# Optimization experiments

Hardware: AMD Instinct MI355X
Metric: run time of the kernel (lower is better)

The kernel has to match this reference:

```python
import jax, jax.numpy as jnp
import numpy as np

D = 2            # n_angles (torus T^2)
NEURONS = 256
EPS = 1e-4       # PD regularizer on inertia matrix / Cholesky diagonal


def setup_inputs() -> dict:
    key = jax.random.key(0)
    ks = jax.random.split(key, 12)
    n = 131072
    d = D
    n_off = d * (d - 1) // 2
    x = jax.random.normal(ks[0], (n, 3 * d), dtype=jnp.float32)
    t = jnp.zeros((), dtype=jnp.float32)

    def lin(k, fan_in, fan_out):
        s = 1.0 / np.sqrt(fan_in)
        kw, kb = jax.random.split(k)
        W = jax.random.uniform(kw, (fan_in, fan_out), jnp.float32, -s, s)
        b = jax.random.uniform(kb, (fan_out,), jnp.float32, -s, s)
        return W, b

    W0, b0 = lin(ks[1], 2 * d, NEURONS)      # trunk layer 1 (input = angle embedding)
    W1, b1 = lin(ks[2], NEURONS, NEURONS)    # trunk layer 2
    Wd, bd = lin(ks[3], NEURONS, d)          # Cholesky diagonal head
    Wo, bo = lin(ks[4], NEURONS, n_off)      # Cholesky off-diagonal head
    Wv, bv = lin(ks[5], NEURONS, 1)          # potential energy head
    return {"t": t, "x": x, "W0": W0, "b0": b0, "W1": W1, "b1": b1,
            "Wd": Wd, "bd": bd, "Wo": Wo, "bo": bo, "Wv": Wv, "bv": bv}


def reference(t, x, W0, b0, W1, b1, Wd, bd, Wo, bo, Wv, bv):
    n = x.shape[0]
    d = x.shape[1] // 3
    q, q_dot, tau = jnp.split(x, [d, 2 * d], axis=1)
    di = jnp.diag_indices(d)
    ti = jnp.tril_indices(d, -1)
    eye = jnp.eye(d, dtype=x.dtype)

    def rigid_body(qi):  # qi: (d,) -> H (d,d) PD, V scalar
        emb = jnp.concatenate([jnp.cos(qi), jnp.sin(qi)])  # angle embedding (2d,)
        h = jnp.tanh(emb @ W0 + b0)
        h = jnp.tanh(h @ W1 + b1)
        l_diag = jax.nn.softplus(h @ Wd + bd) + EPS
        l_off = h @ Wo + bo
        V = (h @ Wv + bv)[0]
        L = jnp.zeros((d, d), x.dtype).at[di].set(l_diag).at[ti].set(l_off)
        H = L @ L.T + EPS * eye
        return H, V

    def dyn(qi, qdi, taui):
        H, _ = rigid_body(qi)
        # Coriolis: dHv/dq @ q_dot - d(0.5 q_dot^T H q_dot)/dq
        Hv_field = jax.jacfwd(lambda qq: rigid_body(qq)[0] @ qdi)(qi)        # (d, d)
        KE_field = jax.grad(lambda qq: 0.5 * qdi @ (rigid_body(qq)[0] @ qdi))(qi)
        C = Hv_field @ qdi - KE_field
        g = jax.grad(lambda qq: rigid_body(qq)[1])(qi)                        # dV/dq
        return jnp.linalg.solve(H, taui - C - g)                              # H qdd = rhs

    q_ddot = jax.vmap(dyn)(q, q_dot, tau)  # (n, d)
    return jnp.concatenate([q_dot, q_ddot, jnp.zeros_like(q_dot)], axis=1)
```

## Files before the change

kernel.cpp:

```cpp
#include <hip/hip_runtime.h>
#include <math.h>

#define SB 32
#define NTHREADS 512

typedef short short8 __attribute__((ext_vector_type(8)));
typedef float f32x4  __attribute__((ext_vector_type(4)));

__device__ __forceinline__ unsigned short f2bf(float f) {
    unsigned int u = __builtin_bit_cast(unsigned int, f);
    unsigned int r = (u + 0x7FFFu + ((u >> 16) & 1u)) >> 16;
    return (unsigned short)r;
}
__device__ __forceinline__ float bf2f(unsigned short h) {
    unsigned int u = ((unsigned int)h) << 16;
    return __builtin_bit_cast(float, u);
}
__device__ __forceinline__ unsigned pack2(unsigned short lo, unsigned short hi) {
    return (unsigned)lo | ((unsigned)hi << 16);
}
__device__ __forceinline__ float softplus_f(float z) {
    return z > 15.f ? z : log1pf(expf(z));
}
__device__ __forceinline__ float fast_tanh(float z) {
    const float e = __builtin_amdgcn_exp2f(z * 2.8853900817779268f);
    return fmaf(-2.f, __builtin_amdgcn_rcpf(e + 1.f), 1.f);
}
__device__ __forceinline__ unsigned selv(bool c, unsigned a, unsigned b) {
    return c ? a : b;
}
__device__ __forceinline__ unsigned sx(unsigned v, int m) {
    return (unsigned)__shfl_xor((int)v, m);
}

__global__ void prep(const float* __restrict__ W1, const float* __restrict__ W0,
                     const float* __restrict__ Wd, const float* __restrict__ Wo,
                     const float* __restrict__ Wv,
                     unsigned short* __restrict__ wB,
                     float4* __restrict__ w0p, float4* __restrict__ hwp)
{
    int idx = blockIdx.x * blockDim.x + threadIdx.x;
    if (idx < 256) {
        w0p[idx] = make_float4(W0[idx], W0[256 + idx], W0[512 + idx], W0[768 + idx]);
        hwp[idx] = make_float4(Wd[2 * idx], Wd[2 * idx + 1], Wo[idx], Wv[idx]);
    }
    if (idx < 8192) {
        const int l  = idx & 63;
        const int ks = (idx >> 6) & 7;
        const int nt = idx >> 9;
        const int k0 = ks * 32 + (l >> 4) * 8;
        const int n  = nt * 16 + (l & 15);
        const int hbase = (nt * 1024 + ks * 64 + l) * 8;
        const int lbase = (nt * 1024 + 512 + ks * 64 + l) * 8;
        #pragma unroll
        for (int i = 0; i < 8; ++i) {
            const float f = W1[(k0 + i) * 256 + n];
            const unsigned short hi = f2bf(f);
            const unsigned short lo = f2bf(f - bf2f(hi));
            wB[hbase + i] = hi;
            wB[lbase + i] = lo;
        }
    }
}

__global__ __launch_bounds__(NTHREADS, 4)
void lode_mfma(const float* __restrict__ x,
               const float4* __restrict__ w0p, const float* __restrict__ b0,
               const unsigned short* __restrict__ wB,
               const float* __restrict__ b1,
               const float4* __restrict__ hwp,
               const float* __restrict__ bd, const float* __restrict__ bo,
               float* __restrict__ out, int n)
{
    __shared__ uint4 S[2048];

    const int tid  = threadIdx.x;
    const int wave = tid >> 6;
    const int lane = tid & 63;
    const int r15  = lane & 15;
    const int s    = r15 & 3;
    const int rho  = r15 >> 2;
    const bool rb0 = (rho & 1) != 0;
    const bool rb1 = (rho & 2) != 0;

    int sg1 = blockIdx.x * SB + wave * 4 + s;
    if (sg1 >= n) sg1 = n - 1;
    const float qq0 = x[sg1 * 6 + 0];
    const float qq1 = x[sg1 * 6 + 1];
    float ss_, cc_;
    sincosf(rb0 ? qq1 : qq0, &ss_, &cc_);
    const float ss_o = __shfl_xor(ss_, 4);
    const float cc_o = __shfl_xor(cc_, 4);
    const float sn0 = rb0 ? ss_o : ss_;
    const float cs0 = rb0 ? cc_o : cc_;
    const float sn1 = rb0 ? ss_ : ss_o;
    const float cs1 = rb0 ? cc_ : cc_o;

    short8 aF[8];
    #pragma unroll
    for (int ks = 0; ks < 8; ++ks) {
        const int kg = lane >> 4;
        const int j0 = ks * 32 + kg * 8 + 2 * rho;
        const float4 wa = w0p[j0];
        const float4 wb = w0p[j0 + 1];
        const float2 bb = *reinterpret_cast<const float2*>(&b0[j0]);
        float z0 = bb.x;
        z0 = fmaf(cs0, wa.x, z0); z0 = fmaf(cs1, wa.y, z0);
        z0 = fmaf(sn0, wa.z, z0); z0 = fmaf(sn1, wa.w, z0);
        float z1 = bb.y;
        z1 = fmaf(cs0, wb.x, z1); z1 = fmaf(cs1, wb.y, z1);
        z1 = fmaf(sn0, wb.z, z1); z1 = fmaf(sn1, wb.w, z1);
        const float h0 = fast_tanh(z0);
        const float h1 = fast_tanh(z1);
        const unsigned short h0h = f2bf(h0);
        const unsigned short h1h = f2bf(h1);
        const unsigned short h0l = f2bf(h0 - bf2f(h0h));
        const unsigned short h1l = f2bf(h1 - bf2f(h1h));
        const float dt0 = fmaf(-h0, h0, 1.f);
        const float dt1 = fmaf(-h1, h1, 1.f);
        const float ta0 = dt0 * fmaf(-sn0, wa.x, cs0 * wa.z);
        const float ta1 = dt1 * fmaf(-sn0, wb.x, cs0 * wb.z);
        const float tb0 = dt0 * fmaf(-sn1, wa.y, cs1 * wa.w);
        const float tb1 = dt1 * fmaf(-sn1, wb.y, cs1 * wb.w);
        const unsigned v0 = pack2(h0h, h1h);
        const unsigned v1 = pack2(h0l, h1l);
        const unsigned v2 = pack2(f2bf(ta0), f2bf(ta1));
        const unsigned v3 = pack2(f2bf(tb0), f2bf(tb1));
        const unsigned s0 = selv(rb1, selv(rb0, v3, v2), selv(rb0, v1, v0));
        const unsigned s1 = selv(rb1, selv(rb0, v2, v3), selv(rb0, v0, v1));
        const unsigned s2 = selv(rb1, selv(rb0, v1, v0), selv(rb0, v3, v2));
        const unsigned s3 = selv(rb1, selv(rb0, v0, v1), selv(rb0, v2, v3));
        const unsigned r4  = sx(s1, 4);
        const unsigned r8  = sx(s2, 8);
        const unsigned r12 = sx(s3, 12);
        const unsigned w0 = selv(rb1, selv(rb0, r12, r8), selv(rb0, r4, s0));
        const unsigned w1 = selv(rb1, selv(rb0, r8, r12), selv(rb0, s0, r4));
        const unsigned w2 = selv(rb1, selv(rb0, r4, s0), selv(rb0, r12, r8));
        const unsigned w3 = selv(rb1, selv(rb0, s0, r4), selv(rb0, r8, r12));
        aF[ks] = __builtin_bit_cast(short8, make_uint4(w0, w1, w2, w3));
    }

    {
        const char* src = (const char*)wB;
        #pragma unroll
        for (int g = 0; g < 2; ++g) {
            const int chunk = wave * 2 + g;
            __builtin_amdgcn_global_load_lds(
                (const __attribute__((address_space(1))) void*)(src + chunk * 1024 + lane * 16),
                (__attribute__((address_space(3))) void*)&S[chunk * 64 + lane], 16, 0, 0);
        }
    }
    __syncthreads();

    float u0[4] = {0,0,0,0}, u1[4] = {0,0,0,0}, u2[4] = {0,0,0,0}, u3[4] = {0,0,0,0};
    const int col = lane & 15;
    const int q   = lane >> 4;
    const bool qb0 = (q & 1) != 0;
    const bool qb1 = (q & 2) != 0;
    const bool qlt2 = (q < 2);

    #pragma unroll 1
    for (int nt = 0; nt < 16; ++nt) {
        {
            const int ntn = (nt + 1) & 15;
            const int bn  = (nt + 1) & 1;
            const char* src = (const char*)wB + ntn * 16384;
            #pragma unroll
            for (int g = 0; g < 2; ++g) {
                const int chunk = wave * 2 + g;
                __builtin_amdgcn_global_load_lds(
                    (const __attribute__((address_space(1))) void*)(src + chunk * 1024 + lane * 16),
                    (__attribute__((address_space(3))) void*)&S[bn * 1024 + chunk * 64 + lane],
                    16, 0, 0);
            }
        }

        const int ncol = nt * 16 + col;
        const float4 hw  = hwp[ncol];
        const float  b1v = b1[ncol];

        const uint4* Bb = &S[(nt & 1) * 1024];
        f32x4 c1 = {0.f,0.f,0.f,0.f};
        f32x4 c2 = {0.f,0.f,0.f,0.f};
        #pragma unroll
        for (int ks = 0; ks < 8; ++ks) {
            const short8 bh = *reinterpret_cast<const short8*>(&Bb[ks * 64 + lane]);
            const short8 bl = *reinterpret_cast<const short8*>(&Bb[512 + ks * 64 + lane]);
            c1 = __builtin_amdgcn_mfma_f32_16x16x32_bf16(aF[ks], bh, c1, 0, 0, 0);
            c2 = __builtin_amdgcn_mfma_f32_16x16x32_bf16(aF[ks], bl, c2, 0, 0, 0);
        }

        float zs[4], zf[4], zA[4];
        #pragma unroll
        for (int r = 0; r < 4; ++r) zs[r] = c1[r] + c2[r];
        #pragma unroll
        for (int r = 0; r < 4; ++r) zf[r] = zs[r] + __shfl_xor(zs[r], 16) + b1v;
        #pragma unroll
        for (int r = 0; r < 4; ++r) {
            const float zr = __shfl_xor(zf[r], 32);
            zA[r] = qlt2 ? zf[r] : zr;
        }
        const float zpick = qb1 ? (qb0 ? zA[3] : zA[2]) : (qb0 ? zA[1] : zA[0]);
        const float hq = fast_tanh(zpick);
        const float g1 = __shfl_xor(hq, 16);
        const float g2 = __shfl_xor(hq, 32);
        const float g3 = __shfl_xor(hq, 48);
        float hr[4];
        hr[0] = qb1 ? (qb0 ? g3 : g2) : (qb0 ? g1 : hq);
        hr[1] = qb1 ? (qb0 ? g2 : g3) : (qb0 ? hq : g1);
        hr[2] = qb1 ? (qb0 ? g1 : hq) : (qb0 ? g3 : g2);
        hr[3] = qb1 ? (qb0 ? hq : g1) : (qb0 ? g2 : g3);
        #pragma unroll
        for (int r = 0; r < 4; ++r) {
            const float dt  = fmaf(-hr[r], hr[r], 1.f);
            const float val = qlt2 ? hr[r] : dt * zs[r];
            u0[r] = fmaf(val, hw.x, u0[r]);
            u1[r] = fmaf(val, hw.y, u1[r]);
            u2[r] = fmaf(val, hw.z, u2[r]);
            u3[r] = fmaf(val, hw.w, u3[r]);
        }
        __syncthreads();
    }

    #pragma unroll
    for (int r = 0; r < 4; ++r) {
        #pragma unroll
        for (int m = 1; m < 16; m <<= 1) {
            u0[r] += __shfl_xor(u0[r], m);
            u1[r] += __shfl_xor(u1[r], m);
            u2[r] += __shfl_xor(u2[r], m);
            u3[r] += __shfl_xor(u3[r], m);
        }
    }
    float pa0[4], pa1[4], pa2[4], pa3[4], pb0[4], pb1[4], pb2[4], pb3[4];
    #pragma unroll
    for (int r = 0; r < 4; ++r) {
        pa0[r] = __shfl_xor(u0[r], 32);
        pa1[r] = __shfl_xor(u1[r], 32);
        pa2[r] = __shfl_xor(u2[r], 32);
        pa3[r] = __shfl_xor(u3[r], 32);
        pb0[r] = __shfl_xor(u0[r], 48);
        pb1[r] = __shfl_xor(u1[r], 48);
        pb2[r] = __shfl_xor(u2[r], 48);
        pb3[r] = __shfl_xor(u3[r], 48);
    }

    if (lane == 0) {
        const float bd0 = bd[0], bd1 = bd[1], bo0 = bo[0];
        #pragma unroll
        for (int r = 0; r < 4; ++r) {
            const int sg = blockIdx.x * SB + wave * 4 + r;
            if (sg < n) {
                const float u    = x[sg * 6 + 2];
                const float vv   = x[sg * 6 + 3];
                const float tau0 = x[sg * 6 + 4];
                const float tau1 = x[sg * 6 + 5];

                const float zd0 = u0[r] + bd0;
                const float zd1 = u1[r] + bd1;
                const float zo  = u2[r] + bo0;

                const float ld0 = softplus_f(zd0) + 1e-4f;
                const float ld1 = softplus_f(zd1) + 1e-4f;
                const float lo  = zo;

                const float sg0 = 1.f / (1.f + expf(-zd0));
                const float sg1 = 1.f / (1.f + expf(-zd1));

                const float pa_d0 = pa0[r], pa_d1 = pa1[r], pa_o = pa2[r], pa_v = pa3[r];
                const float pb_d0 = pb0[r], pb_d1 = pb1[r], pb_o = pb2[r], pb_v = pb3[r];

                const float ld0a = sg0 * pa_d0, ld0b = sg0 * pb_d0;
                const float ld1a = sg1 * pa_d1, ld1b = sg1 * pb_d1;
                const float loa  = pa_o,        lob  = pb_o;
                const float ga   = pa_v,        gb   = pb_v;

                const float H00 = fmaf(ld0, ld0, 1e-4f);
                const float H01 = ld0 * lo;
                const float H11 = fmaf(lo, lo, fmaf(ld1, ld1, 1e-4f));

                const float dH00a = 2.f * ld0 * ld0a, dH00b = 2.f * ld0 * ld0b;
                const float dH01a = fmaf(ld0a, lo, ld0 * loa);
                const float dH01b = fmaf(ld0b, lo, ld0 * lob);
                const float dH11a = 2.f * fmaf(lo, loa, ld1 * ld1a);
                const float dH11b = 2.f * fmaf(lo, lob, ld1 * ld1b);

                const float wa0 = fmaf(dH00a, u, dH01a * vv);
                const float wa1 = fmaf(dH01a, u, dH11a * vv);
                const float wb0 = fmaf(dH00b, u, dH01b * vv);
                const float wb1 = fmaf(dH01b, u, dH11b * vv);

                const float QFa = dH00a*u*u + 2.f*dH01a*u*vv + dH11a*vv*vv;
                const float QFb = dH00b*u*u + 2.f*dH01b*u*vv + dH11b*vv*vv;

                const float C0 = fmaf(wa0, u, wb0 * vv) - 0.5f * QFa;
                const float C1 = fmaf(wa1, u, wb1 * vv) - 0.5f * QFb;

                const float r0 = tau0 - C0 - ga;
                const float r1 = tau1 - C1 - gb;

                const float det = fmaf(H00, H11, -H01 * H01);
                const float inv = 1.f / det;
                const float qdd0 = (H11 * r0 - H01 * r1) * inv;
                const float qdd1 = (H00 * r1 - H01 * r0) * inv;

                float2* o = reinterpret_cast<float2*>(&out[sg * 6]);
                o[0] = make_float2(u, vv);
                o[1] = make_float2(qdd0, qdd1);
                o[2] = make_float2(0.f, 0.f);
            }
        }
    }
}

extern "C" void kernel_launch(void* const* d_in, const int* in_sizes, int n_in,
                              void* d_out, int out_size, void* d_ws, size_t ws_size,
                              hipStream_t stream) {
    const float* x  = (const float*)d_in[1];
    const float* W0 = (const float*)d_in[2];
    const float* b0 = (const float*)d_in[3];
    const float* W1 = (const float*)d_in[4];
    const float* b1 = (const float*)d_in[5];
    const float* Wd = (const float*)d_in[6];
    const float* bd = (const float*)d_in[7];
    const float* Wo = (const float*)d_in[8];
    const float* bo = (const float*)d_in[9];
    const float* Wv = (const float*)d_in[10];
    float* out = (float*)d_out;

    unsigned short* wB = (unsigned short*)d_ws;
    float4* w0p = (float4*)((char*)d_ws + 262144);
    float4* hwp = (float4*)((char*)d_ws + 262144 + 4096);

    const int n = in_sizes[1] / 6;

    prep<<<32, 256, 0, stream>>>(W1, W0, Wd, Wo, Wv, wB, w0p, hwp);

    const int grid = (n + SB - 1) / SB;
    lode_mfma<<<grid, NTHREADS, 0, stream>>>(x, w0p, b0, wB, b1, hwp, bd, bo, out, n);
}
```

Before: 278.5 us.

## Process two sample groups per wave to reuse LDS-loaded W1 fragments

Halves the block to 4 waves, with each wave handling 8 samples as two independent groups (A and B) instead of 4. Each W1 B-fragment read from LDS now feeds four MFMAs instead of two, which halves LDS read traffic per sample and gives more independent MFMA chains for latency hiding. The cost is roughly double the register use for A fragments and accumulators (launch bounds drop to 3 blocks per SM) and fewer waves to share the cooperative global-to-LDS weight loads.

```diff
diff --git a/kernel.cpp b/kernel.cpp
--- a/kernel.cpp
+++ b/kernel.cpp
@@ -2,7 +2,7 @@
 #include <math.h>
 
 #define SB 32
-#define NTHREADS 512
+#define NTHREADS 256
 
 typedef short short8 __attribute__((ext_vector_type(8)));
 typedef float f32x4  __attribute__((ext_vector_type(4)));
@@ -63,43 +63,13 @@
     }
 }
 
-__global__ __launch_bounds__(NTHREADS, 4)
-void lode_mfma(const float* __restrict__ x,
-               const float4* __restrict__ w0p, const float* __restrict__ b0,
-               const unsigned short* __restrict__ wB,
-               const float* __restrict__ b1,
-               const float4* __restrict__ hwp,
-               const float* __restrict__ bd, const float* __restrict__ bo,
-               float* __restrict__ out, int n)
-{
-    __shared__ uint4 S[2048];
-
-    const int tid  = threadIdx.x;
-    const int wave = tid >> 6;
-    const int lane = tid & 63;
-    const int r15  = lane & 15;
-    const int s    = r15 & 3;
-    const int rho  = r15 >> 2;
-    const bool rb0 = (rho & 1) != 0;
-    const bool rb1 = (rho & 2) != 0;
-
-    int sg1 = blockIdx.x * SB + wave * 4 + s;
-    if (sg1 >= n) sg1 = n - 1;
-    const float qq0 = x[sg1 * 6 + 0];
-    const float qq1 = x[sg1 * 6 + 1];
-    float ss_, cc_;
-    sincosf(rb0 ? qq1 : qq0, &ss_, &cc_);
-    const float ss_o = __shfl_xor(ss_, 4);
-    const float cc_o = __shfl_xor(cc_, 4);
-    const float sn0 = rb0 ? ss_o : ss_;
-    const float cs0 = rb0 ? cc_o : cc_;
-    const float sn1 = rb0 ? ss_ : ss_o;
-    const float cs1 = rb0 ? cc_ : cc_o;
-
-    short8 aF[8];
+__device__ __forceinline__ void build_aF(
+    const float4* __restrict__ w0p, const float* __restrict__ b0,
+    int kg, int rho, bool rb0, bool rb1,
+    float sn0, float cs0, float sn1, float cs1, short8* aF)
+{
     #pragma unroll
     for (int ks = 0; ks < 8; ++ks) {
-        const int kg = lane >> 4;
         const int j0 = ks * 32 + kg * 8 + 2 * rho;
         const float4 wa = w0p[j0];
         const float4 wb = w0p[j0 + 1];
@@ -139,12 +109,155 @@
         const unsigned w3 = selv(rb1, selv(rb0, s0, r4), selv(rb0, r8, r12));
         aF[ks] = __builtin_bit_cast(short8, make_uint4(w0, w1, w2, w3));
     }
+}
+
+__device__ __forceinline__ void epi_acc(
+    const f32x4& c1, const f32x4& c2, float b1v, const float4& hw,
+    bool qb0, bool qb1, bool qlt2,
+    float* u0, float* u1, float* u2, float* u3)
+{
+    float zs[4], zf[4], zA[4];
+    #pragma unroll
+    for (int r = 0; r < 4; ++r) zs[r] = c1[r] + c2[r];
+    #pragma unroll
+    for (int r = 0; r < 4; ++r) zf[r] = zs[r] + __shfl_xor(zs[r], 16) + b1v;
+    #pragma unroll
+    for (int r = 0; r < 4; ++r) {
+        const float zr = __shfl_xor(zf[r], 32);
+        zA[r] = qlt2 ? zf[r] : zr;
+    }
+    const float zpick = qb1 ? (qb0 ? zA[3] : zA[2]) : (qb0 ? zA[1] : zA[0]);
+    const float hq = fast_tanh(zpick);
+    const float g1 = __shfl_xor(hq, 16);
+    const float g2 = __shfl_xor(hq, 32);
+    const float g3 = __shfl_xor(hq, 48);
+    float hr[4];
+    hr[0] = qb1 ? (qb0 ? g3 : g2) : (qb0 ? g1 : hq);
+    hr[1] = qb1 ? (qb0 ? g2 : g3) : (qb0 ? hq : g1);
+    hr[2] = qb1 ? (qb0 ? g1 : hq) : (qb0 ? g3 : g2);
+    hr[3] = qb1 ? (qb0 ? hq : g1) : (qb0 ? g2 : g3);
+    #pragma unroll
+    for (int r = 0; r < 4; ++r) {
+        const float dt  = fmaf(-hr[r], hr[r], 1.f);
+        const float val = qlt2 ? hr[r] : dt * zs[r];
+        u0[r] = fmaf(val, hw.x, u0[r]);
+        u1[r] = fmaf(val, hw.y, u1[r]);
+        u2[r] = fmaf(val, hw.z, u2[r]);
+        u3[r] = fmaf(val, hw.w, u3[r]);
+    }
+}
+
+__device__ __forceinline__ void solve_write(
+    const float* __restrict__ x, float* __restrict__ out, int sg,
+    float phd0, float phd1, float phoo,
+    float pad0, float pad1, float pao, float pav,
+    float pbd0, float pbd1, float pbo, float pbv,
+    float bd0, float bd1, float bo0)
+{
+    const float u    = x[sg * 6 + 2];
+    const float vv   = x[sg * 6 + 3];
+    const float tau0 = x[sg * 6 + 4];
+    const float tau1 = x[sg * 6 + 5];
+
+    const float zd0 = phd0 + bd0;
+    const float zd1 = phd1 + bd1;
+    const float zo  = phoo + bo0;
+
+    const float ld0 = softplus_f(zd0) + 1e-4f;
+    const float ld1 = softplus_f(zd1) + 1e-4f;
+    const float lo  = zo;
+
+    const float sg0 = 1.f / (1.f + expf(-zd0));
+    const float sg1 = 1.f / (1.f + expf(-zd1));
+
+    const float ld0a = sg0 * pad0, ld0b = sg0 * pbd0;
+    const float ld1a = sg1 * pad1, ld1b = sg1 * pbd1;
+    const float loa  = pao,        lob  = pbo;
+    const float ga   = pav,        gb   = pbv;
+
+    const float H00 = fmaf(ld0, ld0, 1e-4f);
+    const float H01 = ld0 * lo;
+    const float H11 = fmaf(lo, lo, fmaf(ld1, ld1, 1e-4f));
+
+    const float dH00a = 2.f * ld0 * ld0a, dH00b = 2.f * ld0 * ld0b;
+    const float dH01a = fmaf(ld0a, lo, ld0 * loa);
+    const float dH01b = fmaf(ld0b, lo, ld0 * lob);
+    const float dH11a = 2.f * fmaf(lo, loa, ld1 * ld1a);
+    const float dH11b = 2.f * fmaf(lo, lob, ld1 * ld1b);
+
+    const float wa0 = fmaf(dH00a, u, dH01a * vv);
+    const float wa1 = fmaf(dH01a, u, dH11a * vv);
+    const float wb0 = fmaf(dH00b, u, dH01b * vv);
+    const float wb1 = fmaf(dH01b, u, dH11b * vv);
+
+    const float QFa = dH00a*u*u + 2.f*dH01a*u*vv + dH11a*vv*vv;
+    const float QFb = dH00b*u*u + 2.f*dH01b*u*vv + dH11b*vv*vv;
+
+    const float C0 = fmaf(wa0, u, wb0 * vv) - 0.5f * QFa;
+    const float C1 = fmaf(wa1, u, wb1 * vv) - 0.5f * QFb;
+
+    const float r0 = tau0 - C0 - ga;
+    const float r1 = tau1 - C1 - gb;
+
+    const float det = fmaf(H00, H11, -H01 * H01);
+    const float inv = 1.f / det;
+    const float qdd0 = (H11 * r0 - H01 * r1) * inv;
+    const float qdd1 = (H00 * r1 - H01 * r0) * inv;
+
+    float2* o = reinterpret_cast<float2*>(&out[sg * 6]);
+    o[0] = make_float2(u, vv);
+    o[1] = make_float2(qdd0, qdd1);
+    o[2] = make_float2(0.f, 0.f);
+}
+
+__global__ __launch_bounds__(NTHREADS, 3)
+void lode_mfma(const float* __restrict__ x,
+               const float4* __restrict__ w0p, const float* __restrict__ b0,
+               const unsigned short* __restrict__ wB,
+               const float* __restrict__ b1,
+               const float4* __restrict__ hwp,
+               const float* __restrict__ bd, const float* __restrict__ bo,
+               float* __restrict__ out, int n)
+{
+    __shared__ uint4 S[2048];
+
+    const int tid  = threadIdx.x;
+    const int wave = tid >> 6;
+    const int lane = tid & 63;
+    const int r15  = lane & 15;
+    const int s    = r15 & 3;
+    const int rho  = r15 >> 2;
+    const bool rb0 = (rho & 1) != 0;
+    const bool rb1 = (rho & 2) != 0;
+    const int kg   = lane >> 4;
+
+    int sgA = blockIdx.x * SB + wave * 8 + s;
+    int sgB = sgA + 4;
+    if (sgA >= n) sgA = n - 1;
+    if (sgB >= n) sgB = n - 1;
+    const float qA0 = x[sgA * 6 + 0];
+    const float qA1 = x[sgA * 6 + 1];
+    const float qB0 = x[sgB * 6 + 0];
+    const float qB1 = x[sgB * 6 + 1];
+    float ssA, ccA, ssB, ccB;
+    sincosf(rb0 ? qA1 : qA0, &ssA, &ccA);
+    sincosf(rb0 ? qB1 : qB0, &ssB, &ccB);
+    const float ssAo = __shfl_xor(ssA, 4), ccAo = __shfl_xor(ccA, 4);
+    const float ssBo = __shfl_xor(ssB, 4), ccBo = __shfl_xor(ccB, 4);
+    const float snA0 = rb0 ? ssAo : ssA, csA0 = rb0 ? ccAo : ccA;
+    const float snA1 = rb0 ? ssA : ssAo, csA1 = rb0 ? ccA : ccAo;
+    const float snB0 = rb0 ? ssBo : ssB, csB0 = rb0 ? ccBo : ccB;
+    const float snB1 = rb0 ? ssB : ssBo, csB1 = rb0 ? ccB : ccBo;
+
+    short8 aFA[8], aFB[8];
+    build_aF(w0p, b0, kg, rho, rb0, rb1, snA0, csA0, snA1, csA1, aFA);
+    build_aF(w0p, b0, kg, rho, rb0, rb1, snB0, csB0, snB1, csB1, aFB);
 
     {
         const char* src = (const char*)wB;
         #pragma unroll
-        for (int g = 0; g < 2; ++g) {
-            const int chunk = wave * 2 + g;
+        for (int g = 0; g < 4; ++g) {
+            const int chunk = g * 4 + wave;
             __builtin_amdgcn_global_load_lds(
                 (const __attribute__((address_space(1))) void*)(src + chunk * 1024 + lane * 16),
                 (__attribute__((address_space(3))) void*)&S[chunk * 64 + lane], 16, 0, 0);
@@ -152,7 +265,8 @@
     }
     __syncthreads();
 
-    float u0[4] = {0,0,0,0}, u1[4] = {0,0,0,0}, u2[4] = {0,0,0,0}, u3[4] = {0,0,0,0};
+    float uA0[4] = {0,0,0,0}, uA1[4] = {0,0,0,0}, uA2[4] = {0,0,0,0}, uA3[4] = {0,0,0,0};
+    float uB0[4] = {0,0,0,0}, uB1[4] = {0,0,0,0}, uB2[4] = {0,0,0,0}, uB3[4] = {0,0,0,0};
     const int col = lane & 15;
     const int q   = lane >> 4;
     const bool qb0 = (q & 1) != 0;
@@ -166,8 +280,8 @@
             const int bn  = (nt + 1) & 1;
             const char* src = (const char*)wB + ntn * 16384;
             #pragma unroll
-            for (int g = 0; g < 2; ++g) {
-                const int chunk = wave * 2 + g;
+            for (int g = 0; g < 4; ++g) {
+                const int chunk = g * 4 + wave;
                 __builtin_amdgcn_global_load_lds(
                     (const __attribute__((address_space(1))) void*)(src + chunk * 1024 + lane * 16),
                     (__attribute__((address_space(3))) void*)&S[bn * 1024 + chunk * 64 + lane],
@@ -180,45 +294,20 @@
         const float  b1v = b1[ncol];
 
         const uint4* Bb = &S[(nt & 1) * 1024];
-        f32x4 c1 = {0.f,0.f,0.f,0.f};
-        f32x4 c2 = {0.f,0.f,0.f,0.f};
+        f32x4 c1A = {0.f,0.f,0.f,0.f}, c2A = {0.f,0.f,0.f,0.f};
+        f32x4 c1B = {0.f,0.f,0.f,0.f}, c2B = {0.f,0.f,0.f,0.f};
         #pragma unroll
         for (int ks = 0; ks < 8; ++ks) {
             const short8 bh = *reinterpret_cast<const short8*>(&Bb[ks * 64 + lane]);
             const short8 bl = *reinterpret_cast<const short8*>(&Bb[512 + ks * 64 + lane]);
-            c1 = __builtin_amdgcn_mfma_f32_16x16x32_bf16(aF[ks], bh, c1, 0, 0, 0);
-            c2 = __builtin_amdgcn_mfma_f32_16x16x32_bf16(aF[ks], bl, c2, 0, 0, 0);
-        }
-
-        float zs[4], zf[4], zA[4];
-        #pragma unroll
-        for (int r = 0; r < 4; ++r) zs[r] = c1[r] + c2[r];
-        #pragma unroll
-        for (int r = 0; r < 4; ++r) zf[r] = zs[r] + __shfl_xor(zs[r], 16) + b1v;
-        #pragma unroll
-        for (int r = 0; r < 4; ++r) {
-            const float zr = __shfl_xor(zf[r], 32);
-            zA[r] = qlt2 ? zf[r] : zr;
-        }
-        const float zpick = qb1 ? (qb0 ? zA[3] : zA[2]) : (qb0 ? zA[1] : zA[0]);
-        const float hq = fast_tanh(zpick);
-        const float g1 = __shfl_xor(hq, 16);
-        const float g2 = __shfl_xor(hq, 32);
-        const float g3 = __shfl_xor(hq, 48);
-        float hr[4];
-        hr[0] = qb1 ? (qb0 ? g3 : g2) : (qb0 ? g1 : hq);
-        hr[1] = qb1 ? (qb0 ? g2 : g3) : (qb0 ? hq : g1);
-        hr[2] = qb1 ? (qb0 ? g1 : hq) : (qb0 ? g3 : g2);
-        hr[3] = qb1 ? (qb0 ? hq : g1) : (qb0 ? g2 : g3);
-        #pragma unroll
-        for (int r = 0; r < 4; ++r) {
-            const float dt  = fmaf(-hr[r], hr[r], 1.f);
-            const float val = qlt2 ? hr[r] : dt * zs[r];
-            u0[r] = fmaf(val, hw.x, u0[r]);
-            u1[r] = fmaf(val, hw.y, u1[r]);
-            u2[r] = fmaf(val, hw.z, u2[r]);
-            u3[r] = fmaf(val, hw.w, u3[r]);
-        }
+            c1A = __builtin_amdgcn_mfma_f32_16x16x32_bf16(aFA[ks], bh, c1A, 0, 0, 0);
+            c2A = __builtin_amdgcn_mfma_f32_16x16x32_bf16(aFA[ks], bl, c2A, 0, 0, 0);
+            c1B = __builtin_amdgcn_mfma_f32_16x16x32_bf16(aFB[ks], bh, c1B, 0, 0, 0);
+            c2B = __builtin_amdgcn_mfma_f32_16x16x32_bf16(aFB[ks], bl, c2B, 0, 0, 0);
+        }
+
+        epi_acc(c1A, c2A, b1v, hw, qb0, qb1, qlt2, uA0, uA1, uA2, uA3);
+        epi_acc(c1B, c2B, b1v, hw, qb0, qb1, qlt2, uB0, uB1, uB2, uB3);
         __syncthreads();
     }
 
@@ -226,89 +315,53 @@
     for (int r = 0; r < 4; ++r) {
         #pragma unroll
         for (int m = 1; m < 16; m <<= 1) {
-            u0[r] += __shfl_xor(u0[r], m);
-            u1[r] += __shfl_xor(u1[r], m);
-            u2[r] += __shfl_xor(u2[r], m);
-            u3[r] += __shfl_xor(u3[r], m);
-        }
-    }
-    float pa0[4], pa1[4], pa2[4], pa3[4], pb0[4], pb1[4], pb2[4], pb3[4];
+            uA0[r] += __shfl_xor(uA0[r], m);
+            uA1[r] += __shfl_xor(uA1[r], m);
+            uA2[r] += __shfl_xor(uA2[r], m);
+            uA3[r] += __shfl_xor(uA3[r], m);
+            uB0[r] += __shfl_xor(uB0[r], m);
+            uB1[r] += __shfl_xor(uB1[r], m);
+            uB2[r] += __shfl_xor(uB2[r], m);
+            uB3[r] += __shfl_xor(uB3[r], m);
+        }
+    }
+    float paA0[4], paA1[4], paA2[4], paA3[4], pbA0[4], pbA1[4], pbA2[4], pbA3[4];
+    float paB0[4], paB1[4], paB2[4], paB3[4], pbB0[4], pbB1[4], pbB2[4], pbB3[4];
     #pragma unroll
     for (int r = 0; r < 4; ++r) {
-        pa0[r] = __shfl_xor(u0[r], 32);
-        pa1[r] = __shfl_xor(u1[r], 32);
-        pa2[r] = __shfl_xor(u2[r], 32);
-        pa3[r] = __shfl_xor(u3[r], 32);
-        pb0[r] = __shfl_xor(u0[r], 48);
-        pb1[r] = __shfl_xor(u1[r], 48);
-        pb2[r] = __shfl_xor(u2[r], 48);
-        pb3[r] = __shfl_xor(u3[r], 48);
+        paA0[r] = __shfl_xor(uA0[r], 32);
+        paA1[r] = __shfl_xor(uA1[r], 32);
+        paA2[r] = __shfl_xor(uA2[r], 32);
+        paA3[r] = __shfl_xor(uA3[r], 32);
+        pbA0[r] = __shfl_xor(uA0[r], 48);
+        pbA1[r] = __shfl_xor(uA1[r], 48);
+        pbA2[r] = __shfl_xor(uA2[r], 48);
+        pbA3[r] = __shfl_xor(uA3[r], 48);
+        paB0[r] = __shfl_xor(uB0[r], 32);
+        paB1[r] = __shfl_xor(uB1[r], 32);
+        paB2[r] = __shfl_xor(uB2[r], 32);
+        paB3[r] = __shfl_xor(uB3[r], 32);
+        pbB0[r] = __shfl_xor(uB0[r], 48);
+        pbB1[r] = __shfl_xor(uB1[r], 48);
+        pbB2[r] = __shfl_xor(uB2[r], 48);
+        pbB3[r] = __shfl_xor(uB3[r], 48);
     }
 
     if (lane == 0) {
         const float bd0 = bd[0], bd1 = bd[1], bo0 = bo[0];
+        const int base = blockIdx.x * SB + wave * 8;
         #pragma unroll
         for (int r = 0; r < 4; ++r) {
-            const int sg = blockIdx.x * SB + wave * 4 + r;
-            if (sg < n) {
-                const float u    = x[sg * 6 + 2];
-                const float vv   = x[sg * 6 + 3];
-                const float tau0 = x[sg * 6 + 4];
-                const float tau1 = x[sg * 6 + 5];
-
-                const float zd0 = u0[r] + bd0;
-                const float zd1 = u1[r] + bd1;
-                const float zo  = u2[r] + bo0;
-
-                const float ld0 = softplus_f(zd0) + 1e-4f;
-                const float ld1 = softplus_f(zd1) + 1e-4f;
-                const float lo  = zo;
-
-                const float sg0 = 1.f / (1.f + expf(-zd0));
-                const float sg1 = 1.f / (1.f + expf(-zd1));
-
-                const float pa_d0 = pa0[r], pa_d1 = pa1[r], pa_o = pa2[r], pa_v = pa3[r];
-                const float pb_d0 = pb0[r], pb_d1 = pb1[r], pb_o = pb2[r], pb_v = pb3[r];
-
-                const float ld0a = sg0 * pa_d0, ld0b = sg0 * pb_d0;
-                const float ld1a = sg1 * pa_d1, ld1b = sg1 * pb_d1;
-                const float loa  = pa_o,        lob  = pb_o;
-                const float ga   = pa_v,        gb   = pb_v;
-
-                const float H00 = fmaf(ld0, ld0, 1e-4f);
-                const float H01 = ld0 * lo;
-                const float H11 = fmaf(lo, lo, fmaf(ld1, ld1, 1e-4f));
-
-                const float dH00a = 2.f * ld0 * ld0a, dH00b = 2.f * ld0 * ld0b;
-                const float dH01a = fmaf(ld0a, lo, ld0 * loa);
-                const float dH01b = fmaf(ld0b, lo, ld0 * lob);
-                const float dH11a = 2.f * fmaf(lo, loa, ld1 * ld1a);
-                const float dH11b = 2.f * fmaf(lo, lob, ld1 * ld1b);
-
-                const float wa0 = fmaf(dH00a, u, dH01a * vv);
-                const float wa1 = fmaf(dH01a, u, dH11a * vv);
-                const float wb0 = fmaf(dH00b, u, dH01b * vv);
-                const float wb1 = fmaf(dH01b, u, dH11b * vv);
-
-                const float QFa = dH00a*u*u + 2.f*dH01a*u*vv + dH11a*vv*vv;
-                const float QFb = dH00b*u*u + 2.f*dH01b*u*vv + dH11b*vv*vv;
-
-                const float C0 = fmaf(wa0, u, wb0 * vv) - 0.5f * QFa;
-                const float C1 = fmaf(wa1, u, wb1 * vv) - 0.5f * QFb;
-
-                const float r0 = tau0 - C0 - ga;
-                const float r1 = tau1 - C1 - gb;
-
-                const float det = fmaf(H00, H11, -H01 * H01);
-                const float inv = 1.f / det;
-                const float qdd0 = (H11 * r0 - H01 * r1) * inv;
-                const float qdd1 = (H00 * r1 - H01 * r0) * inv;
-
-                float2* o = reinterpret_cast<float2*>(&out[sg * 6]);
-                o[0] = make_float2(u, vv);
-                o[1] = make_float2(qdd0, qdd1);
-                o[2] = make_float2(0.f, 0.f);
-            }
+            if (base + r < n)
+                solve_write(x, out, base + r,
+                            uA0[r], uA1[r], uA2[r],
+                            paA0[r], paA1[r], paA2[r], paA3[r],
+                            pbA0[r], pbA1[r], pbA2[r], pbA3[r], bd0, bd1, bo0);
+            if (base + 4 + r < n)
+                solve_write(x, out, base + 4 + r,
+                            uB0[r], uB1[r], uB2[r],
+                            paB0[r], paB1[r], paB2[r], paB3[r],
+                            pbB0[r], pbB1[r], pbB2[r], pbB3[r], bd0, bd1, bo0);
         }
     }
 }
```

Measured after the change: 278.4 us. No clear change (-0.0%).
